# Kernel optimization log

Measured on AMD Instinct MI355X. Metric: run time of the kernel, lower is better.

Reference implementation:

```python
import jax, jax.numpy as jnp
import numpy as np

BETA = 0.95
THR = 1.0  # snntorch Leaky default threshold

# Heaviside spike with ATan surrogate gradient (snntorch default, alpha=2):
# d/dx = 1 / (1 + (pi*x)^2)
@jax.custom_vjp
def spike_fn(x):
    return (x > 0).astype(x.dtype)

def _spike_fwd(x):
    return spike_fn(x), x

def _spike_bwd(x, g):
    return (g / (1.0 + (jnp.pi * x) ** 2),)

spike_fn.defvjp(_spike_fwd, _spike_bwd)


def setup_inputs() -> dict:
    key = jax.random.key(0)
    ks = jax.random.split(key, 5)
    T, B, D_in, D_h, D_out = 25, 4096, 784, 1000, 10
    x = jax.random.normal(ks[0], (T, B, D_in), dtype=jnp.float32)
    # Kaiming-uniform-ish init like nn.Linear
    w1 = jax.random.uniform(ks[1], (D_h, D_in), jnp.float32, -1, 1) / np.sqrt(D_in)
    b1 = jax.random.uniform(ks[2], (D_h,), jnp.float32, -1, 1) / np.sqrt(D_in)
    w2 = jax.random.uniform(ks[3], (D_out, D_h), jnp.float32, -1, 1) / np.sqrt(D_h)
    b2 = jax.random.uniform(ks[4], (D_out,), jnp.float32, -1, 1) / np.sqrt(D_h)
    return {"x": x, "w1": w1, "b1": b1, "w2": w2, "b2": b2}


def reference(x, w1, b1, w2, b2):
    B = x.shape[1]
    mem1_0 = jnp.zeros((B, w1.shape[0]), x.dtype)
    mem2_0 = jnp.zeros((B, w2.shape[0]), x.dtype)

    def step(carry, xt):
        mem1, mem2 = carry
        # layer 1: Linear + Leaky (reset-by-subtraction, reset from prior mem)
        cur1 = xt @ w1.T + b1
        reset1 = spike_fn(mem1 - THR)
        mem1 = BETA * mem1 + cur1 - reset1 * THR
        spk1 = spike_fn(mem1 - THR)
        # layer 2
        cur2 = spk1 @ w2.T + b2
        reset2 = spike_fn(mem2 - THR)
        mem2 = BETA * mem2 + cur2 - reset2 * THR
        spk2 = spike_fn(mem2 - THR)
        return (mem1, mem2), spk2

    (mem1, mem2), spk_rec = jax.lax.scan(step, (mem1_0, mem2_0), x)
    return spk_rec, mem2
```

## Files before the change

### kernel.cpp

```cpp
#include <hip/hip_runtime.h>

typedef _Float16 f16;
typedef _Float16 f16x4 __attribute__((ext_vector_type(4)));
typedef _Float16 f16x8 __attribute__((ext_vector_type(8)));
typedef float f32x4 __attribute__((ext_vector_type(4)));

#define T_STEPS 25
#define BATCH   4096
#define DIN     784
#define DH      1000
#define HP      1024
#define DOUT    10
#define MROWS   (T_STEPS * BATCH)
#define KSEG    800
#define KA      (2 * KSEG)
#define KB      (3 * KSEG)
#define WROW    2432
#define NT64    38

__global__ void prep_kernel(const float* __restrict__ x, const float* __restrict__ w1,
                            const float* __restrict__ b1, const float* __restrict__ w2,
                            f16* __restrict__ Ah, f16* __restrict__ Wh,
                            float* __restrict__ b1p, float* __restrict__ w2t)
{
    const int stride = gridDim.x * blockDim.x;
    const int tid0 = blockIdx.x * blockDim.x + threadIdx.x;

    const int total = MROWS * 200;
    for (int idx = tid0; idx < total; idx += stride) {
        const int r  = idx / 200;
        const int c4 = (idx - r * 200) * 4;
        f16x4 hi, lo;
        if (c4 < DIN) {
            const float4 v = *(const float4*)(x + (size_t)r * DIN + c4);
            const float vv[4] = {v.x, v.y, v.z, v.w};
            #pragma unroll
            for (int j = 0; j < 4; ++j) {
                f16 h = (f16)vv[j];
                hi[j] = h;
                lo[j] = (f16)(vv[j] - (float)h);
            }
        } else {
            #pragma unroll
            for (int j = 0; j < 4; ++j) { hi[j] = (f16)0.f; lo[j] = (f16)0.f; }
        }
        *(f16x4*)(Ah + (size_t)r * KA + c4)        = hi;
        *(f16x4*)(Ah + (size_t)r * KA + KSEG + c4) = lo;
    }

    for (int idx = tid0; idx < HP * WROW; idx += stride) {
        const int n  = idx / WROW;
        const int k  = idx - n * WROW;
        f16 v = (f16)0.f;
        if (k < KB) {
            const int seg = k / KSEG;
            const int kc  = k - seg * KSEG;
            float w = (n < DH && kc < DIN) ? w1[n * DIN + kc] : 0.f;
            f16 h = (f16)w;
            v = (seg < 2) ? h : (f16)(w - (float)h);
        }
        Wh[idx] = v;
    }
    for (int idx = tid0; idx < HP; idx += stride)
        b1p[idx] = (idx < DH) ? b1[idx] : 0.f;
    for (int idx = tid0; idx < HP * DOUT; idx += stride) {
        const int h = idx / DOUT;
        const int o = idx - h * DOUT;
        w2t[idx] = (h < DH) ? w2[o * DH + h] : 0.f;
    }
}

#define GL(gp, ldsoff) __builtin_amdgcn_global_load_lds( \
    (const __attribute__((address_space(1))) void*)(gp), \
    (__attribute__((address_space(3))) void*)(lds + (ldsoff)), 16, 0, 0)

#define STAGE64(tt) do { \
    const int _buf = ((tt) & 1) * 8192; \
    const int _ak  = (((tt) < 25) ? (tt) : ((tt) - 25)) * 64; \
    const int _bk  = (tt) * 64; \
    GL(Ag + _ak + 0 * 64 * KA,   _buf + 0 * 4096 + widoff); \
    GL(Ag + _ak + 1 * 64 * KA,   _buf + 1 * 4096 + widoff); \
    GL(Bg + _bk + 0 * 64 * WROW, 16384 + _buf + 0 * 4096 + widoff); \
    GL(Bg + _bk + 1 * 64 * WROW, 16384 + _buf + 1 * 4096 + widoff); } while (0)

#define MFMA8(A0, A1, A2, A3, B0, B1) \
    acc[0][0] = __builtin_amdgcn_mfma_f32_16x16x32_f16(A0, B0, acc[0][0], 0, 0, 0); \
    acc[0][1] = __builtin_amdgcn_mfma_f32_16x16x32_f16(A0, B1, acc[0][1], 0, 0, 0); \
    acc[1][0] = __builtin_amdgcn_mfma_f32_16x16x32_f16(A1, B0, acc[1][0], 0, 0, 0); \
    acc[1][1] = __builtin_amdgcn_mfma_f32_16x16x32_f16(A1, B1, acc[1][1], 0, 0, 0); \
    acc[2][0] = __builtin_amdgcn_mfma_f32_16x16x32_f16(A2, B0, acc[2][0], 0, 0, 0); \
    acc[2][1] = __builtin_amdgcn_mfma_f32_16x16x32_f16(A2, B1, acc[2][1], 0, 0, 0); \
    acc[3][0] = __builtin_amdgcn_mfma_f32_16x16x32_f16(A3, B0, acc[3][0], 0, 0, 0); \
    acc[3][1] = __builtin_amdgcn_mfma_f32_16x16x32_f16(A3, B1, acc[3][1], 0, 0, 0);

#define RD(off) (*(const f16x8*)(lds + (off)))
#define LGKM(n) asm volatile("s_waitcnt lgkmcnt(" #n ")" ::: "memory")
#define SB      __builtin_amdgcn_sched_barrier(0)
#define P1      __builtin_amdgcn_s_setprio(1)
#define P0      __builtin_amdgcn_s_setprio(0)

#define BODY64(tt, STG) do { \
    const int bufc = ((tt) & 1) * 8192; \
    f16x8 a00, a01, a02, a03, b00, b01; \
    f16x8 a10, a11, a12, a13, b10, b11; \
    if (STG) STAGE64((tt) + 1); \
    b00 = RD(bbase + bufc + 0 * 1024 + cA0); \
    b01 = RD(bbase + bufc + 1 * 1024 + cA0); \
    a00 = RD(abase + bufc + 0 * 1024 + cA0); \
    a01 = RD(abase + bufc + 1 * 1024 + cA0); \
    a02 = RD(abase + bufc + 2 * 1024 + cA0); \
    a03 = RD(abase + bufc + 3 * 1024 + cA0); \
    b10 = RD(bbase + bufc + 0 * 1024 + cA1); \
    b11 = RD(bbase + bufc + 1 * 1024 + cA1); \
    a10 = RD(abase + bufc + 0 * 1024 + cA1); \
    a11 = RD(abase + bufc + 1 * 1024 + cA1); \
    a12 = RD(abase + bufc + 2 * 1024 + cA1); \
    a13 = RD(abase + bufc + 3 * 1024 + cA1); \
    LGKM(6); SB;                                   \
    P1; MFMA8(a00, a01, a02, a03, b00, b01) P0; \
    LGKM(0); SB;                                   \
    P1; MFMA8(a10, a11, a12, a13, b10, b11) P0; \
    if (STG) { \
        asm volatile("s_waitcnt vmcnt(0)" ::: "memory"); \
        __builtin_amdgcn_s_barrier(); \
    } \
} while (0)

__global__ __launch_bounds__(512, 4)
void gemm_kernel(const f16* __restrict__ A, const f16* __restrict__ B,
                 const float* __restrict__ bias, float* __restrict__ C)
{
    __shared__ f16 lds[32768];

    const int bid = blockIdx.x;
    const int swz = (bid & 7) * 800 + (bid >> 3);
    const int mt = swz >> 3;
    const int nt = swz & 7;
    const size_t rowBase = (size_t)mt * 128;
    const int colBase = nt * 128;

    const int tid  = threadIdx.x;
    const int wid  = tid >> 6;
    const int lane = tid & 63;
    const int wm = wid >> 2;
    const int wn = wid & 3;

    const int gsw = (tid & 7) ^ ((tid >> 3) & 7);
    const f16* Ag = A + (rowBase + (tid >> 3)) * KA + gsw * 8;
    const f16* Bg = B + (size_t)(colBase + (tid >> 3)) * WROW + gsw * 8;
    const int widoff = wid * 512;

    const int cA0 = (((lane >> 4))     ^ (lane & 7)) * 8;
    const int cA1 = (((lane >> 4) + 4) ^ (lane & 7)) * 8;
    const int abase = (wm * 64 + (lane & 15)) * 64;
    const int bbase = 16384 + (wn * 32 + (lane & 15)) * 64;

    f32x4 acc[4][2];
    #pragma unroll
    for (int m = 0; m < 4; ++m)
        #pragma unroll
        for (int n = 0; n < 2; ++n)
            acc[m][n] = (f32x4){0.f, 0.f, 0.f, 0.f};

    STAGE64(0);
    asm volatile("s_waitcnt vmcnt(0)" ::: "memory");
    __builtin_amdgcn_s_barrier();

    for (int t = 0; t < NT64 - 1; ++t)
        BODY64(t, 1);
    BODY64(NT64 - 1, 0);

    const int c_col0 = colBase + wn * 32 + (lane & 15);
    const size_t c_row0 = rowBase + wm * 64 + (lane >> 4) * 4;
    #pragma unroll
    for (int n = 0; n < 2; ++n) {
        const int gcol = c_col0 + n * 16;
        const float bv = bias[gcol];
        #pragma unroll
        for (int m = 0; m < 4; ++m) {
            const size_t grow = c_row0 + m * 16;
            #pragma unroll
            for (int r = 0; r < 4; ++r)
                C[(grow + r) * HP + gcol] = acc[m][n][r] + bv;
        }
    }
}

__global__ __launch_bounds__(256)
void phase2_kernel(const float* __restrict__ cur1, const float* __restrict__ w2t,
                   const float* __restrict__ b2, float* __restrict__ out)
{
    __shared__ float w2s[HP * DOUT];
    const int tid = threadIdx.x;
    for (int i = tid; i < HP * DOUT; i += 256) w2s[i] = w2t[i];

    const int lane = tid & 63;
    const int wave = tid >> 6;
    const int b = blockIdx.x * 4 + wave;

    float m1[16];
    #pragma unroll
    for (int i = 0; i < 16; ++i) m1[i] = 0.f;
    float m2[DOUT], b2r[DOUT];
    #pragma unroll
    for (int o = 0; o < DOUT; ++o) { m2[o] = 0.f; b2r[o] = b2[o]; }
    __syncthreads();

    for (int t = 0; t < T_STEPS; ++t) {
        const float* cr = cur1 + ((size_t)t * BATCH + b) * HP;
        float p[DOUT];
        #pragma unroll
        for (int o = 0; o < DOUT; ++o) p[o] = 0.f;

        #pragma unroll
        for (int c = 0; c < 4; ++c) {
            const float4 cu = *(const float4*)(cr + c * 256 + lane * 4);
            const float cv[4] = {cu.x, cu.y, cu.z, cu.w};
            #pragma unroll
            for (int j = 0; j < 4; ++j) {
                const float mo = m1[c * 4 + j];
                const float rs = (mo > 1.0f) ? 1.0f : 0.0f;
                const float mn = 0.95f * mo + cv[j] - rs;
                m1[c * 4 + j] = mn;
                if (mn > 1.0f) {
                    const float* wr = w2s + (c * 256 + lane * 4 + j) * DOUT;
                    #pragma unroll
                    for (int o = 0; o < DOUT; ++o) p[o] += wr[o];
                }
            }
        }
        #pragma unroll
        for (int o = 0; o < DOUT; ++o) {
            float v = p[o];
            #pragma unroll
            for (int msk = 32; msk > 0; msk >>= 1) v += __shfl_xor(v, msk, 64);
            p[o] = v;
        }
        #pragma unroll
        for (int o = 0; o < DOUT; ++o) {
            const float cur2 = p[o] + b2r[o];
            const float mo = m2[o];
            const float rs = (mo > 1.0f) ? 1.0f : 0.0f;
            m2[o] = 0.95f * mo + cur2 - rs;
        }
        if (lane < DOUT)
            out[(size_t)t * (BATCH * DOUT) + (size_t)b * DOUT + lane] =
                (m2[lane] > 1.0f) ? 1.0f : 0.0f;
    }
    if (lane < DOUT)
        out[(size_t)T_STEPS * BATCH * DOUT + (size_t)b * DOUT + lane] = m2[lane];
}

extern "C" void kernel_launch(void* const* d_in, const int* in_sizes, int n_in,
                              void* d_out, int out_size, void* d_ws, size_t ws_size,
                              hipStream_t stream)
{
    const float* x  = (const float*)d_in[0];
    const float* w1 = (const float*)d_in[1];
    const float* b1 = (const float*)d_in[2];
    const float* w2 = (const float*)d_in[3];
    const float* b2 = (const float*)d_in[4];
    float* out = (float*)d_out;

    char* wsb = (char*)d_ws;
    f16*   Ah   = (f16*)(wsb);
    f16*   Wh   = (f16*)(wsb + 327680000);
    float* cur1 = (float*)(wsb + 327680000 + 4980736);
    float* b1p  = (float*)(wsb + 327680000 + 4980736 + 419430400);
    float* w2t  = (float*)(wsb + 327680000 + 4980736 + 419430400 + 4096);

    prep_kernel<<<4096, 256, 0, stream>>>(x, w1, b1, w2, Ah, Wh, b1p, w2t);
    gemm_kernel<<<6400, 512, 0, stream>>>(Ah, Wh, b1p, cur1);
    phase2_kernel<<<1024, 256, 0, stream>>>(cur1, w2t, b2, out);
}
```

Before: 805.0 us.

## Restructure GEMM to 4 waves with 64x64 warp tiles and K=32 stages

The GEMM block drops from 8 waves to 4, and each wave now computes a 64x64 sub-tile (4x4 MFMAs) instead of 64x32. The K step per stage halves from 64 to 32, which halves LDS use and needs a new swizzled load/read layout. The goal is more MFMA work per LDS fragment read and more blocks resident per CU. In exchange, barriers per K are doubled, register pressure is higher, and the shorter stages give less room to hide latency.

Result: slower. 1.027 ms (+27.5%).

```diff
diff --git a/kernel.cpp b/kernel.cpp
--- a/kernel.cpp
+++ b/kernel.cpp
@@ -16,7 +16,7 @@
 #define KA      (2 * KSEG)
 #define KB      (3 * KSEG)
 #define WROW    2432
-#define NT64    38
+#define NT32    76
 
 __global__ void prep_kernel(const float* __restrict__ x, const float* __restrict__ w1,
                             const float* __restrict__ b1, const float* __restrict__ w2,
@@ -74,24 +74,32 @@
     (const __attribute__((address_space(1))) void*)(gp), \
     (__attribute__((address_space(3))) void*)(lds + (ldsoff)), 16, 0, 0)
 
-#define STAGE64(tt) do { \
-    const int _buf = ((tt) & 1) * 8192; \
-    const int _ak  = (((tt) < 25) ? (tt) : ((tt) - 25)) * 64; \
-    const int _bk  = (tt) * 64; \
-    GL(Ag + _ak + 0 * 64 * KA,   _buf + 0 * 4096 + widoff); \
-    GL(Ag + _ak + 1 * 64 * KA,   _buf + 1 * 4096 + widoff); \
-    GL(Bg + _bk + 0 * 64 * WROW, 16384 + _buf + 0 * 4096 + widoff); \
-    GL(Bg + _bk + 1 * 64 * WROW, 16384 + _buf + 1 * 4096 + widoff); } while (0)
-
-#define MFMA8(A0, A1, A2, A3, B0, B1) \
+#define STAGE32(tt) do { \
+    const int _buf = ((tt) & 1) * 4096; \
+    const int _ak  = (((tt) < 50) ? (tt) : ((tt) - 50)) * 32; \
+    const int _bk  = (tt) * 32; \
+    GL(Ag + _ak,            _buf + 0 * 2048 + widoff); \
+    GL(Ag + _ak + 64 * KA,  _buf + 1 * 2048 + widoff); \
+    GL(Bg + _bk,            8192 + _buf + 0 * 2048 + widoff); \
+    GL(Bg + _bk + 64 * WROW, 8192 + _buf + 1 * 2048 + widoff); } while (0)
+
+#define MFMA16(A0, A1, A2, A3, B0, B1, B2, B3) \
     acc[0][0] = __builtin_amdgcn_mfma_f32_16x16x32_f16(A0, B0, acc[0][0], 0, 0, 0); \
     acc[0][1] = __builtin_amdgcn_mfma_f32_16x16x32_f16(A0, B1, acc[0][1], 0, 0, 0); \
+    acc[0][2] = __builtin_amdgcn_mfma_f32_16x16x32_f16(A0, B2, acc[0][2], 0, 0, 0); \
+    acc[0][3] = __builtin_amdgcn_mfma_f32_16x16x32_f16(A0, B3, acc[0][3], 0, 0, 0); \
     acc[1][0] = __builtin_amdgcn_mfma_f32_16x16x32_f16(A1, B0, acc[1][0], 0, 0, 0); \
     acc[1][1] = __builtin_amdgcn_mfma_f32_16x16x32_f16(A1, B1, acc[1][1], 0, 0, 0); \
+    acc[1][2] = __builtin_amdgcn_mfma_f32_16x16x32_f16(A1, B2, acc[1][2], 0, 0, 0); \
+    acc[1][3] = __builtin_amdgcn_mfma_f32_16x16x32_f16(A1, B3, acc[1][3], 0, 0, 0); \
     acc[2][0] = __builtin_amdgcn_mfma_f32_16x16x32_f16(A2, B0, acc[2][0], 0, 0, 0); \
     acc[2][1] = __builtin_amdgcn_mfma_f32_16x16x32_f16(A2, B1, acc[2][1], 0, 0, 0); \
+    acc[2][2] = __builtin_amdgcn_mfma_f32_16x16x32_f16(A2, B2, acc[2][2], 0, 0, 0); \
+    acc[2][3] = __builtin_amdgcn_mfma_f32_16x16x32_f16(A2, B3, acc[2][3], 0, 0, 0); \
     acc[3][0] = __builtin_amdgcn_mfma_f32_16x16x32_f16(A3, B0, acc[3][0], 0, 0, 0); \
-    acc[3][1] = __builtin_amdgcn_mfma_f32_16x16x32_f16(A3, B1, acc[3][1], 0, 0, 0);
+    acc[3][1] = __builtin_amdgcn_mfma_f32_16x16x32_f16(A3, B1, acc[3][1], 0, 0, 0); \
+    acc[3][2] = __builtin_amdgcn_mfma_f32_16x16x32_f16(A3, B2, acc[3][2], 0, 0, 0); \
+    acc[3][3] = __builtin_amdgcn_mfma_f32_16x16x32_f16(A3, B3, acc[3][3], 0, 0, 0);
 
 #define RD(off) (*(const f16x8*)(lds + (off)))
 #define LGKM(n) asm volatile("s_waitcnt lgkmcnt(" #n ")" ::: "memory")
@@ -99,38 +107,31 @@
 #define P1      __builtin_amdgcn_s_setprio(1)
 #define P0      __builtin_amdgcn_s_setprio(0)
 
-#define BODY64(tt, STG) do { \
-    const int bufc = ((tt) & 1) * 8192; \
-    f16x8 a00, a01, a02, a03, b00, b01; \
-    f16x8 a10, a11, a12, a13, b10, b11; \
-    if (STG) STAGE64((tt) + 1); \
-    b00 = RD(bbase + bufc + 0 * 1024 + cA0); \
-    b01 = RD(bbase + bufc + 1 * 1024 + cA0); \
-    a00 = RD(abase + bufc + 0 * 1024 + cA0); \
-    a01 = RD(abase + bufc + 1 * 1024 + cA0); \
-    a02 = RD(abase + bufc + 2 * 1024 + cA0); \
-    a03 = RD(abase + bufc + 3 * 1024 + cA0); \
-    b10 = RD(bbase + bufc + 0 * 1024 + cA1); \
-    b11 = RD(bbase + bufc + 1 * 1024 + cA1); \
-    a10 = RD(abase + bufc + 0 * 1024 + cA1); \
-    a11 = RD(abase + bufc + 1 * 1024 + cA1); \
-    a12 = RD(abase + bufc + 2 * 1024 + cA1); \
-    a13 = RD(abase + bufc + 3 * 1024 + cA1); \
-    LGKM(6); SB;                                   \
-    P1; MFMA8(a00, a01, a02, a03, b00, b01) P0; \
-    LGKM(0); SB;                                   \
-    P1; MFMA8(a10, a11, a12, a13, b10, b11) P0; \
+#define BODY32(tt, STG) do { \
+    const int bufc = ((tt) & 1) * 4096; \
+    f16x8 a0, a1, a2, a3, b0, b1, b2, b3; \
+    if (STG) STAGE32((tt) + 1); \
+    b0 = RD(bbase + bufc + 0 * 512); \
+    b1 = RD(bbase + bufc + 1 * 512); \
+    b2 = RD(bbase + bufc + 2 * 512); \
+    b3 = RD(bbase + bufc + 3 * 512); \
+    a0 = RD(abase + bufc + 0 * 512); \
+    a1 = RD(abase + bufc + 1 * 512); \
+    a2 = RD(abase + bufc + 2 * 512); \
+    a3 = RD(abase + bufc + 3 * 512); \
+    LGKM(0); SB; \
+    P1; MFMA16(a0, a1, a2, a3, b0, b1, b2, b3) P0; \
     if (STG) { \
         asm volatile("s_waitcnt vmcnt(0)" ::: "memory"); \
         __builtin_amdgcn_s_barrier(); \
     } \
 } while (0)
 
-__global__ __launch_bounds__(512, 4)
+__global__ __launch_bounds__(256, 4)
 void gemm_kernel(const f16* __restrict__ A, const f16* __restrict__ B,
                  const float* __restrict__ bias, float* __restrict__ C)
 {
-    __shared__ f16 lds[32768];
+    __shared__ f16 lds[16384];
 
     const int bid = blockIdx.x;
     const int swz = (bid & 7) * 800 + (bid >> 3);
@@ -142,38 +143,41 @@
     const int tid  = threadIdx.x;
     const int wid  = tid >> 6;
     const int lane = tid & 63;
-    const int wm = wid >> 2;
-    const int wn = wid & 3;
-
-    const int gsw = (tid & 7) ^ ((tid >> 3) & 7);
-    const f16* Ag = A + (rowBase + (tid >> 3)) * KA + gsw * 8;
-    const f16* Bg = B + (size_t)(colBase + (tid >> 3)) * WROW + gsw * 8;
+    const int wm = wid >> 1;
+    const int wn = wid & 1;
+    const int l15 = lane & 15;
+
+    const int q    = (tid & 7) ^ ((tid >> 3) & 7);
+    const int srow = 2 * (tid >> 3) + (q >> 2);
+    const int scol = (q & 3) * 8;
+    const f16* Ag = A + (rowBase + srow) * KA + scol;
+    const f16* Bg = B + (size_t)(colBase + srow) * WROW + scol;
     const int widoff = wid * 512;
 
-    const int cA0 = (((lane >> 4))     ^ (lane & 7)) * 8;
-    const int cA1 = (((lane >> 4) + 4) ^ (lane & 7)) * 8;
-    const int abase = (wm * 64 + (lane & 15)) * 64;
-    const int bbase = 16384 + (wn * 32 + (lane & 15)) * 64;
-
-    f32x4 acc[4][2];
+    const int phys  = ((lane >> 4) + 4 * (lane & 1)) ^ ((l15 >> 1) & 7);
+    const int abase = (wm * 32 + (l15 >> 1)) * 64 + phys * 8;
+    const int bbase = 8192 + (wn * 32 + (l15 >> 1)) * 64 + phys * 8;
+
+    f32x4 acc[4][4];
     #pragma unroll
     for (int m = 0; m < 4; ++m)
         #pragma unroll
-        for (int n = 0; n < 2; ++n)
+        for (int n = 0; n < 4; ++n)
             acc[m][n] = (f32x4){0.f, 0.f, 0.f, 0.f};
 
-    STAGE64(0);
+    STAGE32(0);
     asm volatile("s_waitcnt vmcnt(0)" ::: "memory");
     __builtin_amdgcn_s_barrier();
 
-    for (int t = 0; t < NT64 - 1; ++t)
-        BODY64(t, 1);
-    BODY64(NT64 - 1, 0);
-
-    const int c_col0 = colBase + wn * 32 + (lane & 15);
+    #pragma unroll 4
+    for (int t = 0; t < NT32 - 1; ++t)
+        BODY32(t, 1);
+    BODY32(NT32 - 1, 0);
+
+    const int c_col0 = colBase + wn * 64 + l15;
     const size_t c_row0 = rowBase + wm * 64 + (lane >> 4) * 4;
     #pragma unroll
-    for (int n = 0; n < 2; ++n) {
+    for (int n = 0; n < 4; ++n) {
         const int gcol = c_col0 + n * 16;
         const float bv = bias[gcol];
         #pragma unroll
@@ -270,6 +274,6 @@
     float* w2t  = (float*)(wsb + 327680000 + 4980736 + 419430400 + 4096);
 
     prep_kernel<<<4096, 256, 0, stream>>>(x, w1, b1, w2, Ah, Wh, b1p, w2t);
-    gemm_kernel<<<6400, 512, 0, stream>>>(Ah, Wh, b1p, cur1);
+    gemm_kernel<<<6400, 256, 0, stream>>>(Ah, Wh, b1p, cur1);
     phase2_kernel<<<1024, 256, 0, stream>>>(cur1, w2t, b2, out);
 }
```
